# Kernel tuning notes

Measured on AMD Instinct MI355X. Metric: run time of the kernel, lower is better.

The kernel has to match this reference:

```python
import jax, jax.numpy as jnp
import numpy as np

B, SQ, FDIM = 32, 196, 2048
L, EDIM, H = 1000, 1024, 16
DH = EDIM // H  # 64


def setup_inputs() -> dict:
    key = jax.random.key(0)
    ks = jax.random.split(key, 10)
    s = lambda fan_in: 1.0 / np.sqrt(fan_in)
    return {
        "features": jax.random.normal(ks[0], (B, SQ, FDIM), jnp.float32),
        "label_embeddings": jax.random.normal(ks[1], (L, EDIM), jnp.float32),
        "Wq": jax.random.normal(ks[2], (EDIM, FDIM), jnp.float32) * s(FDIM),
        "bq": jax.random.normal(ks[3], (EDIM,), jnp.float32) * s(FDIM),
        "Wk": jax.random.normal(ks[4], (EDIM, EDIM), jnp.float32) * s(EDIM),
        "bk": jax.random.normal(ks[5], (EDIM,), jnp.float32) * s(EDIM),
        "Wv": jax.random.normal(ks[6], (EDIM, EDIM), jnp.float32) * s(EDIM),
        "bv": jax.random.normal(ks[7], (EDIM,), jnp.float32) * s(EDIM),
        "Wo": jax.random.normal(ks[8], (EDIM, EDIM), jnp.float32) * s(EDIM),
        "bo": jax.random.normal(ks[9], (EDIM,), jnp.float32) * s(EDIM),
    }


def reference(features, label_embeddings, Wq, bq, Wk, bk, Wv, bv, Wo, bo):
    # Q projection: [B, Sq, E] -> [B, Sq, H, Dh]
    q = (jnp.einsum("bsf,ef->bse", features, Wq) + bq).reshape(B, SQ, H, DH)
    # K/V projections on the shared label table: [L, E] -> [L, H, Dh]
    k = (label_embeddings @ Wk.T + bk).reshape(L, H, DH)
    v = (label_embeddings @ Wv.T + bv).reshape(L, H, DH)
    # scores: [B, H, Sq, L]
    scores = jnp.einsum("bqhd,lhd->bhql", q, k) / jnp.sqrt(jnp.float32(DH))
    attn = jax.nn.softmax(scores, axis=-1)
    # attention output: [B, Sq, H, Dh] -> [B, Sq, E]
    ctx = jnp.einsum("bhql,lhd->bqhd", attn, v).reshape(B, SQ, EDIM)
    return jnp.einsum("bse,oe->bso", ctx, Wo) + bo
```

## Files before the change

### kernel.cpp

```cpp
#include <hip/hip_runtime.h>
#include <hip/hip_bf16.h>
#include <stdint.h>
#include <math.h>

constexpr int BB   = 32;
constexpr int SQ   = 196;
constexpr int FDIM = 2048;
constexpr int LL   = 1000;
constexpr int EDIM = 1024;
constexpr int HH   = 16;
constexpr int BSQ  = BB * SQ;

typedef unsigned short u16;
typedef unsigned int   u32;
typedef __attribute__((ext_vector_type(4)))  float f32x4;
typedef __attribute__((ext_vector_type(16))) float f32x16;
typedef __attribute__((ext_vector_type(8)))  short bf16x8;
typedef __attribute__((ext_vector_type(2)))  int   i32x2;

#define DEV __device__ __forceinline__

DEV u16 f2bf(float f) {
  unsigned u = __float_as_uint(f);
  unsigned r = 0x7FFFu + ((u >> 16) & 1u);
  return (u16)((u + r) >> 16);
}

DEV u32 pack2bf(float a, float b) {
  __hip_bfloat162 h = __float22bfloat162_rn(float2{a, b});
  return *reinterpret_cast<const u32*>(&h);
}

#if __has_builtin(__builtin_amdgcn_exp2f)
#define EXP2F(x) __builtin_amdgcn_exp2f(x)
#else
#define EXP2F(x) exp2f(x)
#endif

DEV f32x16 zero16() {
  f32x16 v;
#pragma unroll
  for (int i = 0; i < 16; ++i) v[i] = 0.f;
  return v;
}

#if __has_builtin(__builtin_amdgcn_permlane32_swap)
DEV void half_swap(u32& a, u32& b, int ) {
  i32x2 r = __builtin_amdgcn_permlane32_swap((int)a, (int)b, false, false);
  a = (u32)r[0]; b = (u32)r[1];
}
#else
DEV void half_swap(u32& a, u32& b, int hi) {
  const u32 sa = __shfl_xor(a, 32), sb = __shfl_xor(b, 32);
  const u32 na = hi ? sb : a;
  const u32 nb = hi ? b : sa;
  a = na; b = nb;
}
#endif

#define GLDS16(g, l) __builtin_amdgcn_global_load_lds(                         \
    (const __attribute__((address_space(1))) void*)(g),                       \
    (__attribute__((address_space(3))) void*)(l), 16, 0, 0)

DEV int xcd_chunk(int bid, int cpx) { return (bid & 7) * cpx + (bid >> 3); }

DEV void kv_body(u16* sA, u16* sB, int nb,
                 const float* __restrict__ lab,
                 const float* B1, const float* bias1, u16* C1,
                 const float* B2, const float* bias2, u16* C2) {
  const int tn = nb % 16;
  const int tm = nb / 16;
  const float* Bp; const float* biasp; u16* Cp; int tnl; bool tw;
  if (tn < 8) { Bp = B1; biasp = bias1; Cp = C1; tnl = tn; tw = false; }
  else        { Bp = B2; biasp = bias2; Cp = C2; tnl = tn - 8; tw = true; }

  const int lane = threadIdx.x & 63;
  const int wid  = threadIdx.x >> 6;
  const int wr   = wid >> 1, wc = wid & 1;
  const int lr   = lane & 15, lg = lane >> 4;

  f32x4 acc[4][4];
#pragma unroll
  for (int m = 0; m < 4; ++m)
#pragma unroll
    for (int n = 0; n < 4; ++n) acc[m][n] = (f32x4){0.f, 0.f, 0.f, 0.f};

  for (int k0 = 0; k0 < EDIM; k0 += 64) {
#pragma unroll
    for (int i = 0; i < 4; ++i) {
      const int chunk = wid * 4 + i;
      const int row   = chunk * 8 + (lane >> 3);
      int ga = tm * 128 + row; ga = ga < LL ? ga : LL - 1;
      const size_t ao = (size_t)ga * EDIM + k0 + (lane & 7) * 8;
      const float4 a0 = *reinterpret_cast<const float4*>(lab + ao);
      const float4 a1 = *reinterpret_cast<const float4*>(lab + ao + 4);
      uint4 wa;
      wa.x = pack2bf(a0.x, a0.y); wa.y = pack2bf(a0.z, a0.w);
      wa.z = pack2bf(a1.x, a1.y); wa.w = pack2bf(a1.z, a1.w);
      *reinterpret_cast<uint4*>(&sA[chunk * 512 + lane * 8]) = wa;
      const size_t bo = (size_t)(tnl * 128 + row) * EDIM + k0 + (lane & 7) * 8;
      const float4 b0 = *reinterpret_cast<const float4*>(Bp + bo);
      const float4 b1 = *reinterpret_cast<const float4*>(Bp + bo + 4);
      uint4 wb;
      wb.x = pack2bf(b0.x, b0.y); wb.y = pack2bf(b0.z, b0.w);
      wb.z = pack2bf(b1.x, b1.y); wb.w = pack2bf(b1.z, b1.w);
      *reinterpret_cast<uint4*>(&sB[chunk * 512 + lane * 8]) = wb;
    }
    __syncthreads();
#pragma unroll
    for (int ks = 0; ks < 2; ++ks) {
      bf16x8 af[4], bfr[4];
#pragma unroll
      for (int m = 0; m < 4; ++m)
        af[m] = *reinterpret_cast<const bf16x8*>(&sA[(wr * 64 + m * 16 + lr) * 64 + ks * 32 + lg * 8]);
#pragma unroll
      for (int n = 0; n < 4; ++n)
        bfr[n] = *reinterpret_cast<const bf16x8*>(&sB[(wc * 64 + n * 16 + lr) * 64 + ks * 32 + lg * 8]);
#pragma unroll
      for (int m = 0; m < 4; ++m)
#pragma unroll
        for (int n = 0; n < 4; ++n)
          acc[m][n] = __builtin_amdgcn_mfma_f32_16x16x32_bf16(af[m], bfr[n], acc[m][n], 0, 0, 0);
    }
    __syncthreads();
  }

#pragma unroll
  for (int n = 0; n < 4; ++n) {
    const int c  = tnl * 128 + wc * 64 + n * 16 + lr;
    const float bv = biasp[c];
#pragma unroll
    for (int m = 0; m < 4; ++m) {
#pragma unroll
      for (int r = 0; r < 4; ++r) {
        const int rr = tm * 128 + wr * 64 + m * 16 + lg * 4 + r;
        const float v = acc[m][n][r] + bv;
        if (tw)
          Cp[(size_t)c * 1024 + rr] = (rr < LL) ? f2bf(v) : (u16)0;
        else if (rr < LL)
          Cp[(size_t)rr * 1024 + c] = f2bf(v);
      }
    }
  }
}

constexpr int P_N0 = BSQ * FDIM / 4;
constexpr int P_N1 = P_N0 + EDIM * FDIM / 4;
constexpr int P_N2 = P_N1 + EDIM * EDIM / 4;
constexpr int PREP_GRID = 2048;

__global__ __launch_bounds__(256)
void prep_kernel(const float* __restrict__ lab,
                 const float* __restrict__ wk, const float* __restrict__ bk, u16* ko,
                 const float* __restrict__ wv, const float* __restrict__ bv, u16* vto,
                 const float* __restrict__ f, const float* __restrict__ wq,
                 const float* __restrict__ wo,
                 u16* df, u16* dwq, u16* dwo) {
  __shared__ __attribute__((aligned(16))) u16 sA[128 * 64];
  __shared__ __attribute__((aligned(16))) u16 sB[128 * 64];
  const int bid = blockIdx.x;
  if (bid < 128) {
    int nb = xcd_chunk(bid, 16);
    nb = (nb % 8) * 16 + (nb / 8);
    kv_body(sA, sB, nb, lab, wk, bk, ko, wv, bv, vto);
  } else {
    int i = (bid - 128) * 256 + threadIdx.x;
    const int st = (PREP_GRID - 128) * 256;
    for (; i < P_N2; i += st) {
      const float* s; u16* d; int j;
      if (i < P_N0)      { s = f;  d = df;  j = i; }
      else if (i < P_N1) { s = wq; d = dwq; j = i - P_N0; }
      else               { s = wo; d = dwo; j = i - P_N1; }
      float4 v = reinterpret_cast<const float4*>(s)[j];
      ushort4 o;
      o.x = f2bf(v.x); o.y = f2bf(v.y); o.z = f2bf(v.z); o.w = f2bf(v.w);
      reinterpret_cast<ushort4*>(d)[j] = o;
    }
  }
}

template<bool OUT_BF16>
DEV void body64(const u16* __restrict__ A, const u16* __restrict__ B,
                const float* __restrict__ bias, void* __restrict__ C,
                int K, float scale) {
  __shared__ __attribute__((aligned(16))) u16 sA[64 * 64];
  __shared__ __attribute__((aligned(16))) u16 sB[128 * 64];
  const int nb = xcd_chunk(blockIdx.x, 98);
  const int tn = nb % 8, tm = nb / 8;

  const int lane = threadIdx.x & 63;
  const int wid  = threadIdx.x >> 6;
  const int lr = lane & 15, lg = lane >> 4;

  f32x4 acc[4][2];
#pragma unroll
  for (int m = 0; m < 4; ++m)
#pragma unroll
    for (int n = 0; n < 2; ++n) acc[m][n] = (f32x4){0.f, 0.f, 0.f, 0.f};

  for (int k0 = 0; k0 < K; k0 += 64) {
#pragma unroll
    for (int i = 0; i < 2; ++i) {
      const int chunk = wid * 2 + i;
      const int row = chunk * 8 + (lane >> 3);
      GLDS16(A + (size_t)(tm * 64 + row) * K + k0 + (lane & 7) * 8, &sA[chunk * 512]);
    }
#pragma unroll
    for (int i = 0; i < 4; ++i) {
      const int chunk = wid * 4 + i;
      const int row = chunk * 8 + (lane >> 3);
      GLDS16(B + (size_t)(tn * 128 + row) * K + k0 + (lane & 7) * 8, &sB[chunk * 512]);
    }
    asm volatile("s_waitcnt vmcnt(0)" ::: "memory");
    __syncthreads();
#pragma unroll
    for (int ks = 0; ks < 2; ++ks) {
      bf16x8 af[4], bfr[2];
#pragma unroll
      for (int m = 0; m < 4; ++m)
        af[m] = *reinterpret_cast<const bf16x8*>(&sA[(m * 16 + lr) * 64 + ks * 32 + lg * 8]);
#pragma unroll
      for (int n = 0; n < 2; ++n)
        bfr[n] = *reinterpret_cast<const bf16x8*>(&sB[(wid * 32 + n * 16 + lr) * 64 + ks * 32 + lg * 8]);
#pragma unroll
      for (int m = 0; m < 4; ++m)
#pragma unroll
        for (int n = 0; n < 2; ++n)
          acc[m][n] = __builtin_amdgcn_mfma_f32_16x16x32_bf16(af[m], bfr[n], acc[m][n], 0, 0, 0);
    }
    __syncthreads();
  }

#pragma unroll
  for (int n = 0; n < 2; ++n) {
    const int c = tn * 128 + wid * 32 + n * 16 + lr;
    const float bv = bias[c];
#pragma unroll
    for (int m = 0; m < 4; ++m) {
#pragma unroll
      for (int r = 0; r < 4; ++r) {
        const int rr = tm * 64 + m * 16 + lg * 4 + r;
        const float v = (acc[m][n][r] + bv) * scale;
        if (OUT_BF16) ((u16*)C)[(size_t)rr * 1024 + c] = f2bf(v);
        else          ((float*)C)[(size_t)rr * 1024 + c] = v;
      }
    }
  }
}

__global__ __launch_bounds__(256)
void gemm_qproj(const u16* A, const u16* B, const float* bias, u16* C, float qscale) {
  body64<true>(A, B, bias, C, FDIM, qscale);
}

__global__ __launch_bounds__(256)
void gemm_oproj(const u16* A, const u16* B, const float* bias, float* C) {
  body64<false>(A, B, bias, C, EDIM, 1.0f);
}

__global__ __launch_bounds__(256, 2)
void attn_kernel(const u16* __restrict__ Q, const u16* __restrict__ Kb,
                 const u16* __restrict__ VT, u16* __restrict__ ctx) {
  const int wg = xcd_chunk(blockIdx.x, 98);
  const int h = wg / 49, qb = wg % 49;
  __shared__ __attribute__((aligned(16))) u16 sm[16384];

  const int t    = threadIdx.x;
  const int lane = t & 63;
  const int wid  = t >> 6;
  const int l31  = lane & 31, hi = lane >> 5;

  const int qrow = qb * 128 + wid * 32 + l31;
  const u16* qp = Q + (size_t)qrow * EDIM + h * 64;
  bf16x8 qf[4];
#pragma unroll
  for (int ks = 0; ks < 4; ++ks)
    qf[ks] = *reinterpret_cast<const bf16x8*>(qp + ks * 16 + hi * 8);

  f32x16 ctxa[2]; ctxa[0] = zero16(); ctxa[1] = zero16();
  float lsum = 0.f;

  auto stage = [&](int buf, int l0s) {
#pragma unroll
    for (int i = 0; i < 2; ++i) {
      const int chunk = wid * 2 + i;
      const int row   = chunk * 8 + (lane >> 3);
      const int sl    = (lane & 7) ^ (row & 7);
      int lk = l0s + row; if (lk > LL - 1) lk = LL - 1;
      GLDS16(Kb + (size_t)lk * EDIM + h * 64 + sl * 8, sm + buf * 4096 + chunk * 512);
      GLDS16(VT + (size_t)(h * 64 + row) * 1024 + l0s + sl * 8, sm + 8192 + buf * 4096 + chunk * 512);
    }
  };
  auto frag = [&](const u16* base, int row, int slot) -> bf16x8 {
    return *reinterpret_cast<const bf16x8*>(base + row * 64 + ((slot ^ (row & 7)) * 8));
  };

  constexpr int NT = (LL + 63) / 64;
  stage(0, 0);
  asm volatile("s_waitcnt vmcnt(0)" ::: "memory");
  __syncthreads();

  for (int it = 0; it < NT; ++it) {
    const int l0  = it * 64;
    const int cur = it & 1;
    if (it + 1 < NT) stage(cur ^ 1, l0 + 64);

    const u16* sKb = sm + cur * 4096;
    const u16* sVb = sm + 8192 + cur * 4096;

    f32x16 st[2]; st[0] = zero16(); st[1] = zero16();
    __builtin_amdgcn_s_setprio(1);
#pragma unroll
    for (int ks = 0; ks < 4; ++ks) {
#pragma unroll
      for (int jt = 0; jt < 2; ++jt) {
        bf16x8 kf = frag(sKb, jt * 32 + l31, 2 * ks + hi);
        st[jt] = __builtin_amdgcn_mfma_f32_32x32x16_bf16(kf, qf[ks], st[jt], 0, 0, 0);
      }
    }
    __builtin_amdgcn_s_setprio(0);

    u32 pk[2][4][2];
    auto softmax_pack = [&](bool tail) {
#pragma unroll
      for (int jt = 0; jt < 2; ++jt) {
#pragma unroll
        for (int g = 0; g < 4; ++g) {
          float p[4];
#pragma unroll
          for (int j = 0; j < 4; ++j) {
            float e = EXP2F(st[jt][g * 4 + j]);
            if (tail) {
              const int kg = l0 + jt * 32 + j + 8 * g + 4 * hi;
              if (kg >= LL) e = 0.f;
            }
            p[j] = e;
            lsum += e;
          }
          pk[jt][g][0] = pack2bf(p[0], p[1]);
          pk[jt][g][1] = pack2bf(p[2], p[3]);
        }
      }
    };
    if (l0 + 64 <= LL) softmax_pack(false); else softmax_pack(true);

    __builtin_amdgcn_s_setprio(1);
#pragma unroll
    for (int ksl = 0; ksl < 4; ++ksl) {
      const int jt = ksl >> 1, e2 = ksl & 1;
      u32 x0 = pk[jt][2 * e2 + 0][0], y0 = pk[jt][2 * e2 + 1][0];
      u32 x1 = pk[jt][2 * e2 + 0][1], y1 = pk[jt][2 * e2 + 1][1];
      half_swap(x0, y0, hi);
      half_swap(x1, y1, hi);
      union { u32 d[4]; bf16x8 v; } pf;
      pf.d[0] = x0; pf.d[1] = x1; pf.d[2] = y0; pf.d[3] = y1;
#pragma unroll
      for (int dt = 0; dt < 2; ++dt) {
        bf16x8 vf = frag(sVb, dt * 32 + l31, 2 * ksl + hi);
        ctxa[dt] = __builtin_amdgcn_mfma_f32_32x32x16_bf16(vf, pf.v, ctxa[dt], 0, 0, 0);
      }
    }
    __builtin_amdgcn_s_setprio(0);

    asm volatile("s_waitcnt vmcnt(0)" ::: "memory");
    __syncthreads();
  }

  float ltot = lsum + __shfl_xor(lsum, 32);
  const float inv = 1.0f / ltot;

  u16* tb = sm;
  const int q = wid * 32 + l31;
#pragma unroll
  for (int dt = 0; dt < 2; ++dt) {
#pragma unroll
    for (int g = 0; g < 4; ++g) {
      u32 w0 = pack2bf(ctxa[dt][g * 4 + 0] * inv, ctxa[dt][g * 4 + 1] * inv);
      u32 w1 = pack2bf(ctxa[dt][g * 4 + 2] * inv, ctxa[dt][g * 4 + 3] * inv);
      const int d2   = dt * 64 + g * 16 + hi * 8;
      const int byte = q * 128 + (d2 ^ ((q & 7) << 4));
      *reinterpret_cast<u32*>(reinterpret_cast<char*>(tb) + byte)     = w0;
      *reinterpret_cast<u32*>(reinterpret_cast<char*>(tb) + byte + 4) = w1;
    }
  }
  __syncthreads();
#pragma unroll
  for (int pass = 0; pass < 4; ++pass) {
    const int row  = pass * 32 + (t >> 3);
    const int srow = qb * 128 + row;
    const int cb = ((t & 7) * 16) ^ ((row & 7) << 4);
    uint4 val = *reinterpret_cast<const uint4*>(reinterpret_cast<const char*>(tb) + row * 128 + cb);
    *reinterpret_cast<uint4*>(ctx + (size_t)srow * EDIM + h * 64 + (t & 7) * 8) = val;
  }
}

extern "C" void kernel_launch(void* const* d_in, const int* in_sizes, int n_in,
                              void* d_out, int out_size, void* d_ws, size_t ws_size,
                              hipStream_t stream) {
  const float* features = (const float*)d_in[0];
  const float* labels   = (const float*)d_in[1];
  const float* Wq = (const float*)d_in[2];
  const float* bq = (const float*)d_in[3];
  const float* Wk = (const float*)d_in[4];
  const float* bk = (const float*)d_in[5];
  const float* Wv = (const float*)d_in[6];
  const float* bv = (const float*)d_in[7];
  const float* Wo = (const float*)d_in[8];
  const float* bo = (const float*)d_in[9];
  float* out = (float*)d_out;

  u16* f_bf   = (u16*)d_ws;
  u16* wq_bf  = f_bf   + (size_t)BSQ  * FDIM;
  u16* wo_bf  = wq_bf  + (size_t)EDIM * FDIM;
  u16* q_bf   = wo_bf  + (size_t)EDIM * EDIM;
  u16* k_bf   = q_bf   + (size_t)BSQ  * EDIM;
  u16* vt_bf  = k_bf   + (size_t)LL   * EDIM;
  u16* ctx_bf = vt_bf  + (size_t)1024 * 1024;

  prep_kernel<<<PREP_GRID, 256, 0, stream>>>(
      labels, Wk, bk, k_bf, Wv, bv, vt_bf,
      features, Wq, Wo, f_bf, wq_bf, wo_bf);

  const float qscale = 0.125f * 1.4426950408889634f;
  gemm_qproj<<<784, 256, 0, stream>>>(f_bf, wq_bf, bq, q_bf, qscale);

  attn_kernel<<<784, 256, 0, stream>>>(q_bf, k_bf, vt_bf, ctx_bf);

  gemm_oproj<<<784, 256, 0, stream>>>(ctx_bf, wo_bf, bo, out);
}
```

Baseline: 172.0 us.

## Move K/V projection blocks from prep kernel into Q-projection GEMM launch

```diff
diff --git a/kernel.cpp b/kernel.cpp
--- a/kernel.cpp
+++ b/kernel.cpp
@@ -63,6 +63,28 @@
     (__attribute__((address_space(3))) void*)(l), 16, 0, 0)
 
 DEV int xcd_chunk(int bid, int cpx) { return (bid & 7) * cpx + (bid >> 3); }
+
+constexpr int P_N0 = BSQ * FDIM / 4;
+constexpr int P_N1 = P_N0 + EDIM * FDIM / 4;
+constexpr int P_N2 = P_N1 + EDIM * EDIM / 4;
+
+__global__ __launch_bounds__(256)
+void cvt_all(const float* __restrict__ f, const float* __restrict__ wq,
+             const float* __restrict__ wo,
+             u16* df, u16* dwq, u16* dwo) {
+  int i = blockIdx.x * blockDim.x + threadIdx.x;
+  const int st = gridDim.x * blockDim.x;
+  for (; i < P_N2; i += st) {
+    const float* s; u16* d; int j;
+    if (i < P_N0)      { s = f;  d = df;  j = i; }
+    else if (i < P_N1) { s = wq; d = dwq; j = i - P_N0; }
+    else               { s = wo; d = dwo; j = i - P_N1; }
+    float4 v = reinterpret_cast<const float4*>(s)[j];
+    ushort4 o;
+    o.x = f2bf(v.x); o.y = f2bf(v.y); o.z = f2bf(v.z); o.w = f2bf(v.w);
+    reinterpret_cast<ushort4*>(d)[j] = o;
+  }
+}
 
 DEV void kv_body(u16* sA, u16* sB, int nb,
                  const float* __restrict__ lab,
@@ -144,47 +166,11 @@
   }
 }
 
-constexpr int P_N0 = BSQ * FDIM / 4;
-constexpr int P_N1 = P_N0 + EDIM * FDIM / 4;
-constexpr int P_N2 = P_N1 + EDIM * EDIM / 4;
-constexpr int PREP_GRID = 2048;
-
-__global__ __launch_bounds__(256)
-void prep_kernel(const float* __restrict__ lab,
-                 const float* __restrict__ wk, const float* __restrict__ bk, u16* ko,
-                 const float* __restrict__ wv, const float* __restrict__ bv, u16* vto,
-                 const float* __restrict__ f, const float* __restrict__ wq,
-                 const float* __restrict__ wo,
-                 u16* df, u16* dwq, u16* dwo) {
-  __shared__ __attribute__((aligned(16))) u16 sA[128 * 64];
-  __shared__ __attribute__((aligned(16))) u16 sB[128 * 64];
-  const int bid = blockIdx.x;
-  if (bid < 128) {
-    int nb = xcd_chunk(bid, 16);
-    nb = (nb % 8) * 16 + (nb / 8);
-    kv_body(sA, sB, nb, lab, wk, bk, ko, wv, bv, vto);
-  } else {
-    int i = (bid - 128) * 256 + threadIdx.x;
-    const int st = (PREP_GRID - 128) * 256;
-    for (; i < P_N2; i += st) {
-      const float* s; u16* d; int j;
-      if (i < P_N0)      { s = f;  d = df;  j = i; }
-      else if (i < P_N1) { s = wq; d = dwq; j = i - P_N0; }
-      else               { s = wo; d = dwo; j = i - P_N1; }
-      float4 v = reinterpret_cast<const float4*>(s)[j];
-      ushort4 o;
-      o.x = f2bf(v.x); o.y = f2bf(v.y); o.z = f2bf(v.z); o.w = f2bf(v.w);
-      reinterpret_cast<ushort4*>(d)[j] = o;
-    }
-  }
-}
-
 template<bool OUT_BF16>
-DEV void body64(const u16* __restrict__ A, const u16* __restrict__ B,
+DEV void body64(u16* sA, u16* sB,
+                const u16* __restrict__ A, const u16* __restrict__ B,
                 const float* __restrict__ bias, void* __restrict__ C,
                 int K, float scale) {
-  __shared__ __attribute__((aligned(16))) u16 sA[64 * 64];
-  __shared__ __attribute__((aligned(16))) u16 sB[128 * 64];
   const int nb = xcd_chunk(blockIdx.x, 98);
   const int tn = nb % 8, tm = nb / 8;
 
@@ -249,13 +235,25 @@
 }
 
 __global__ __launch_bounds__(256)
-void gemm_qproj(const u16* A, const u16* B, const float* bias, u16* C, float qscale) {
-  body64<true>(A, B, bias, C, FDIM, qscale);
+void gemm_qproj_kv(const u16* fA, const u16* wqb, const float* bq, u16* qo, float qscale,
+                   const float* lab,
+                   const float* wk, const float* bk, u16* ko,
+                   const float* wv, const float* bv, u16* vto) {
+  __shared__ __attribute__((aligned(16))) u16 smem[16384];
+  const int bid = blockIdx.x;
+  if (bid < 784) {
+    body64<true>(smem, smem + 4096, fA, wqb, bq, qo, FDIM, qscale);
+  } else {
+    int nb = xcd_chunk(bid - 784, 16);
+    nb = (nb % 8) * 16 + (nb / 8);
+    kv_body(smem, smem + 8192, nb, lab, wk, bk, ko, wv, bv, vto);
+  }
 }
 
 __global__ __launch_bounds__(256)
 void gemm_oproj(const u16* A, const u16* B, const float* bias, float* C) {
-  body64<false>(A, B, bias, C, EDIM, 1.0f);
+  __shared__ __attribute__((aligned(16))) u16 smem[12288];
+  body64<false>(smem, smem + 4096, A, B, bias, C, EDIM, 1.0f);
 }
 
 __global__ __launch_bounds__(256, 2)
@@ -417,12 +415,12 @@
   u16* vt_bf  = k_bf   + (size_t)LL   * EDIM;
   u16* ctx_bf = vt_bf  + (size_t)1024 * 1024;
 
-  prep_kernel<<<PREP_GRID, 256, 0, stream>>>(
-      labels, Wk, bk, k_bf, Wv, bv, vt_bf,
-      features, Wq, Wo, f_bf, wq_bf, wo_bf);
+  cvt_all<<<2048, 256, 0, stream>>>(features, Wq, Wo, f_bf, wq_bf, wo_bf);
 
   const float qscale = 0.125f * 1.4426950408889634f;
-  gemm_qproj<<<784, 256, 0, stream>>>(f_bf, wq_bf, bq, q_bf, qscale);
+  gemm_qproj_kv<<<784 + 128, 256, 0, stream>>>(
+      f_bf, wq_bf, bq, q_bf, qscale,
+      labels, Wk, bk, k_bf, Wv, bv, vt_bf);
 
   attn_kernel<<<784, 256, 0, stream>>>(q_bf, k_bf, vt_bf, ctx_bf);
 
```

Result: no change. 173.5 us (+0.9%).
